# Kernel optimization log

Hardware: AMD Instinct MI355X
Metric: run time of the kernel (lower is better)

## Reference

```python
import jax, jax.numpy as jnp
import numpy as np

NEG_SLOPE = 0.2

def gatv2_conv(x, src, dst, Wl, Wr, att, b, num_nodes):
    # GATv2: e = att . leaky_relu(Wl x_src + Wr x_dst); segment softmax over dst; scatter-add of alpha * Wl x_src
    xl = x @ Wl  # [N, out]
    xr = x @ Wr  # [N, out]
    m = xl[src] + xr[dst]                        # [E, out] edge gather
    e = jax.nn.leaky_relu(m, NEG_SLOPE) @ att    # [E]
    emax = jax.ops.segment_max(e, dst, num_segments=num_nodes)
    ee = jnp.exp(e - emax[dst])
    denom = jax.ops.segment_sum(ee, dst, num_segments=num_nodes)
    alpha = ee / denom[dst]                      # [E]
    out = jax.ops.segment_sum(alpha[:, None] * xl[src], dst, num_segments=num_nodes)
    return out + b

def setup_inputs() -> dict:
    key = jax.random.key(0)
    ks = jax.random.split(key, 24)
    N, E, F, H, B = 40000, 640000, 128, 128, 64
    inp = {
        'x': jax.random.normal(ks[0], (N, F), dtype=jnp.float32),
        'edge_index': jax.random.randint(ks[1], (2, E), 0, N),
        'batch': jnp.sort(jax.random.randint(ks[2], (N,), 0, B)),
        'day': jax.random.randint(ks[3], (B,), 0, 7),
        'hour': jax.random.randint(ks[4], (B,), 0, 24),
    }
    def glorot(k, shape):
        lim = float(np.sqrt(6.0 / (shape[0] + shape[1])))
        return jax.random.uniform(k, shape, jnp.float32, -lim, lim)
    # GATv2 layers (heads=1)
    inp['Wl1'] = glorot(ks[5], (F, H)); inp['Wr1'] = glorot(ks[6], (F, H))
    inp['att1'] = glorot(ks[7], (H, 1))[:, 0]; inp['b1'] = jnp.zeros((H,), jnp.float32)
    inp['Wl2'] = glorot(ks[8], (H, H)); inp['Wr2'] = glorot(ks[9], (H, H))
    inp['att2'] = glorot(ks[10], (H, 1))[:, 0]; inp['b2'] = jnp.zeros((H,), jnp.float32)
    inp['Wl3'] = glorot(ks[11], (H, H)); inp['Wr3'] = glorot(ks[12], (H, H))
    inp['att3'] = glorot(ks[13], (H, 1))[:, 0]; inp['b3'] = jnp.zeros((H,), jnp.float32)
    # embeddings
    inp['day_tab'] = jax.random.normal(ks[14], (7, 64), dtype=jnp.float32)
    inp['hour_tab'] = jax.random.normal(ks[15], (24, 64), dtype=jnp.float32)
    # MLP head (weights stored [in, out])
    inp['W1'] = glorot(ks[16], (256, 256)); inp['bl1'] = jnp.zeros((256,), jnp.float32)
    inp['W2'] = glorot(ks[17], (256, 256)); inp['bl2'] = jnp.zeros((256,), jnp.float32)
    inp['W3'] = glorot(ks[18], (256, 1));   inp['bl3'] = jnp.zeros((1,), jnp.float32)
    return inp

def reference(x, edge_index, batch, day, hour,
              Wl1, Wr1, att1, b1, Wl2, Wr2, att2, b2, Wl3, Wr3, att3, b3,
              day_tab, hour_tab, W1, bl1, W2, bl2, W3, bl3):
    N = x.shape[0]
    B = day.shape[0]
    # add self loops (PyG default add_self_loops=True)
    loops = jnp.arange(N)
    src = jnp.concatenate([edge_index[0], loops])
    dst = jnp.concatenate([edge_index[1], loops])
    h = gatv2_conv(x, src, dst, Wl1, Wr1, att1, b1, N)
    h = jax.nn.relu(h)
    h = gatv2_conv(h, src, dst, Wl2, Wr2, att2, b2, N)
    h = jax.nn.relu(h)
    h = gatv2_conv(h, src, dst, Wl3, Wr3, att3, b3, N)
    # global mean pool over graphs
    sums = jax.ops.segment_sum(h, batch, num_segments=B)
    cnts = jax.ops.segment_sum(jnp.ones((N,), h.dtype), batch, num_segments=B)
    pooled = sums / jnp.maximum(cnts, 1.0)[:, None]      # [B, 128]
    feats = jnp.concatenate([pooled, day_tab[day], hour_tab[hour]], axis=1)  # [B, 256]
    z = jax.nn.relu(feats @ W1 + bl1)
    z = jax.nn.relu(z @ W2 + bl2)
    return z @ W3 + bl3  # [B, 1]
```

## Files before the change

### kernel.cpp

```cpp
#include <hip/hip_runtime.h>
#include <math.h>

#define NEG_SLOPE 0.2f
#define POOL_CHUNKS 8

typedef __attribute__((ext_vector_type(8))) short bf16x8;
typedef __attribute__((ext_vector_type(4))) float f32x4;

__device__ __forceinline__ void split_bf16(float x, short& hi, short& lo) {
    unsigned u = __float_as_uint(x);
    unsigned uh = u & 0xFFFF0000u;
    float r = x - __uint_as_float(uh);
    hi = (short)(uh >> 16);
    lo = (short)(__float_as_uint(r) >> 16);
}

__device__ __forceinline__ unsigned f2bf_rne(float x) {
    unsigned u = __float_as_uint(x);
    return (u + 0x7fffu + ((u >> 16) & 1u)) >> 16;
}

__global__ __launch_bounds__(256, 1) void node_gemm(
    const float* __restrict__ h, const float* __restrict__ Wl,
    const float* __restrict__ Wr, unsigned* __restrict__ xlb,
    float* __restrict__ xr, int N, int nTiles)
{
    const int w   = threadIdx.x >> 6;
    const int l   = threadIdx.x & 63;
    const int l15 = l & 15, lg = l >> 4;

    const float* __restrict__ Wsel = (w < 2) ? Wl : Wr;
    const int cbase = (w & 1) * 64;

    bf16x8 bh[4][4], bl_[4][4];
    #pragma unroll
    for (int ct = 0; ct < 4; ++ct) {
        const int c = cbase + ct * 16 + l15;
        #pragma unroll
        for (int kt = 0; kt < 4; ++kt) {
            #pragma unroll
            for (int i = 0; i < 8; ++i) {
                float v = Wsel[(kt * 32 + lg * 8 + i) * 128 + c];
                short hi, lo; split_bf16(v, hi, lo);
                bh[ct][kt][i] = hi; bl_[ct][kt][i] = lo;
            }
        }
    }

    for (int tile = blockIdx.x; tile < nTiles; tile += gridDim.x) {
        const int row0 = tile * 64;

        f32x4 acc[4][4];
        #pragma unroll
        for (int rt = 0; rt < 4; ++rt)
            #pragma unroll
            for (int ct = 0; ct < 4; ++ct)
                acc[rt][ct] = (f32x4){0.f, 0.f, 0.f, 0.f};

        #pragma unroll
        for (int rt = 0; rt < 4; ++rt) {
            int row = row0 + rt * 16 + l15;
            int rowc = row < N ? row : N - 1;
            bf16x8 ah[4], al[4];
            #pragma unroll
            for (int kt = 0; kt < 4; ++kt) {
                const float4 v0 = *(const float4*)&h[(size_t)rowc * 128 + kt * 32 + lg * 8];
                const float4 v1 = *(const float4*)&h[(size_t)rowc * 128 + kt * 32 + lg * 8 + 4];
                const float vv[8] = {v0.x, v0.y, v0.z, v0.w, v1.x, v1.y, v1.z, v1.w};
                #pragma unroll
                for (int i = 0; i < 8; ++i) {
                    short hi, lo; split_bf16(vv[i], hi, lo);
                    ah[kt][i] = hi; al[kt][i] = lo;
                }
            }
            #pragma unroll
            for (int kt = 0; kt < 4; ++kt) {
                #pragma unroll
                for (int ct = 0; ct < 4; ++ct) {
                    acc[rt][ct] = __builtin_amdgcn_mfma_f32_16x16x32_bf16(
                        ah[kt], bh[ct][kt], acc[rt][ct], 0, 0, 0);
                    acc[rt][ct] = __builtin_amdgcn_mfma_f32_16x16x32_bf16(
                        al[kt], bh[ct][kt], acc[rt][ct], 0, 0, 0);
                    acc[rt][ct] = __builtin_amdgcn_mfma_f32_16x16x32_bf16(
                        ah[kt], bl_[ct][kt], acc[rt][ct], 0, 0, 0);
                }
            }
        }

        if (w < 2) {
            #pragma unroll
            for (int rt = 0; rt < 4; ++rt) {
                #pragma unroll
                for (int ct = 0; ct < 4; ++ct) {
                    #pragma unroll
                    for (int j = 0; j < 4; ++j) {
                        int row = row0 + rt * 16 + lg * 4 + j;
                        unsigned o = f2bf_rne(acc[rt][ct][j]);
                        unsigned pr = (unsigned)__shfl_xor((int)o, 1);
                        if (!(l15 & 1) && row < N) {
                            int cp = (cbase + ct * 16 + l15) >> 1;
                            xlb[(size_t)row * 64 + cp] = o | (pr << 16);
                        }
                    }
                }
            }
        } else {
            #pragma unroll
            for (int rt = 0; rt < 4; ++rt) {
                #pragma unroll
                for (int ct = 0; ct < 4; ++ct) {
                    #pragma unroll
                    for (int j = 0; j < 4; ++j) {
                        int row = row0 + rt * 16 + lg * 4 + j;
                        if (row < N)
                            xr[(size_t)row * 128 + cbase + ct * 16 + l15] = acc[rt][ct][j];
                    }
                }
            }
        }
    }
}

__global__ __launch_bounds__(256) void zero_ints(int* __restrict__ p, int n)
{
    int i = blockIdx.x * blockDim.x + threadIdx.x;
    if (i < n) p[i] = 0;
}

__global__ __launch_bounds__(256) void edge_hist(
    const int* __restrict__ ei, int* __restrict__ deg, int E, int ET)
{
    int eid = blockIdx.x * blockDim.x + threadIdx.x;
    if (eid >= ET) return;
    int dst = (eid < E) ? ei[E + eid] : eid - E;
    atomicAdd(&deg[dst], 1);
}

__global__ __launch_bounds__(256) void scan_block(
    const int* __restrict__ in, int* __restrict__ out_excl,
    int* __restrict__ bsum, int N)
{
    __shared__ int sm[256];
    int t = threadIdx.x, i = blockIdx.x * 256 + t;
    int v = (i < N) ? in[i] : 0;
    sm[t] = v;
    __syncthreads();
    int x = v;
    for (int o = 1; o < 256; o <<= 1) {
        int u = (t >= o) ? sm[t - o] : 0;
        __syncthreads();
        x += u; sm[t] = x;
        __syncthreads();
    }
    if (i < N) out_excl[i] = x - v;
    if (t == 255) bsum[blockIdx.x] = x;
}

__global__ __launch_bounds__(256) void scan_sums(int* __restrict__ bsum, int nb)
{
    __shared__ int sm[256];
    int t = threadIdx.x;
    int v = (t < nb) ? bsum[t] : 0;
    sm[t] = v;
    __syncthreads();
    int x = v;
    for (int o = 1; o < 256; o <<= 1) {
        int u = (t >= o) ? sm[t - o] : 0;
        __syncthreads();
        x += u; sm[t] = x;
        __syncthreads();
    }
    if (t < nb) bsum[t] = x - v;
}

__global__ __launch_bounds__(256) void scan_final(
    const int* __restrict__ excl, const int* __restrict__ bsum,
    int* __restrict__ rowptr, int* __restrict__ cursor, int N, int ET)
{
    int i = blockIdx.x * blockDim.x + threadIdx.x;
    if (i > N) return;
    int v = (i < N) ? (excl[i] + bsum[i >> 8]) : ET;
    rowptr[i] = v;
    if (i < N) cursor[i] = v;
}

__global__ __launch_bounds__(256) void edge_fill(
    const int* __restrict__ ei, int* __restrict__ cursor,
    int* __restrict__ srcs, int E, int ET)
{
    int eid = blockIdx.x * blockDim.x + threadIdx.x;
    if (eid >= ET) return;
    int src, dst;
    if (eid < E) { src = ei[eid]; dst = ei[E + eid]; }
    else { src = dst = eid - E; }
    int pos = atomicAdd(&cursor[dst], 1);
    srcs[pos] = src;
}

__global__ __launch_bounds__(256) void gatv2_aggregate(
    const unsigned* __restrict__ xlb, const float* __restrict__ xr,
    const int* __restrict__ rowptr, const int* __restrict__ srcs,
    const float* __restrict__ att, const float* __restrict__ b,
    float* __restrict__ hout, int N, int do_relu)
{
    int n = blockIdx.x * 4 + (threadIdx.x >> 6);
    if (n >= N) return;
    const int lane = threadIdx.x & 63;
    const int hl = lane & 15;
    const int g  = lane >> 4;

    float xr8[8], at8[8];
    {
        const float4 a0 = *(const float4*)&xr[(size_t)n * 128 + hl * 8];
        const float4 a1 = *(const float4*)&xr[(size_t)n * 128 + hl * 8 + 4];
        xr8[0]=a0.x; xr8[1]=a0.y; xr8[2]=a0.z; xr8[3]=a0.w;
        xr8[4]=a1.x; xr8[5]=a1.y; xr8[6]=a1.z; xr8[7]=a1.w;
        const float4 t0 = *(const float4*)&att[hl * 8];
        const float4 t1 = *(const float4*)&att[hl * 8 + 4];
        at8[0]=t0.x; at8[1]=t0.y; at8[2]=t0.z; at8[3]=t0.w;
        at8[4]=t1.x; at8[5]=t1.y; at8[6]=t1.z; at8[7]=t1.w;
    }

    int r0 = rowptr[n], r1 = rowptr[n + 1];
    float m = -INFINITY, s = 0.f;
    float acc[8];
    #pragma unroll
    for (int c = 0; c < 8; ++c) acc[c] = 0.f;

    auto unpack = [&](const uint4 q, float* vv) {
        unsigned u;
        u = q.x; vv[0] = __uint_as_float(u << 16); vv[1] = __uint_as_float(u & 0xFFFF0000u);
        u = q.y; vv[2] = __uint_as_float(u << 16); vv[3] = __uint_as_float(u & 0xFFFF0000u);
        u = q.z; vv[4] = __uint_as_float(u << 16); vv[5] = __uint_as_float(u & 0xFFFF0000u);
        u = q.w; vv[6] = __uint_as_float(u << 16); vv[7] = __uint_as_float(u & 0xFFFF0000u);
    };
    auto score = [&](const float* vv) -> float {
        float p = 0.f;
        #pragma unroll
        for (int c = 0; c < 8; ++c) {
            float t = vv[c] + xr8[c];
            t = fmaxf(t, NEG_SLOPE * t);
            p += t * at8[c];
        }
        return p;
    };
    auto online = [&](float p, const float* vv) {
        float mn = fmaxf(m, p);
        float f = __expf(m - mn);
        float w = __expf(p - mn);
        s = s * f + w;
        #pragma unroll
        for (int c = 0; c < 8; ++c) acc[c] = acc[c] * f + w * vv[c];
        m = mn;
    };

    int j = r0 + g;
    int sa = (j < r1) ? srcs[j] : 0;
    int sb = (j + 4 < r1) ? srcs[j + 4] : sa;
    for (; j + 4 < r1; j += 8) {
        const uint4 qa = *(const uint4*)&xlb[(size_t)sa * 64 + hl * 4];
        const uint4 qb = *(const uint4*)&xlb[(size_t)sb * 64 + hl * 4];
        int jn0 = (j + 8  < r1) ? j + 8  : j;
        int jn1 = (j + 12 < r1) ? j + 12 : j;
        int sna = srcs[jn0], snb = srcs[jn1];
        float va[8], vb[8];
        unpack(qa, va); unpack(qb, vb);
        float pa = score(va), pb = score(vb);
        #pragma unroll
        for (int off = 1; off < 16; off <<= 1) {
            pa += __shfl_xor(pa, off);
            pb += __shfl_xor(pb, off);
        }
        online(pa, va);
        online(pb, vb);
        sa = sna; sb = snb;
    }
    if (j < r1) {
        const uint4 qa = *(const uint4*)&xlb[(size_t)sa * 64 + hl * 4];
        float va[8];
        unpack(qa, va);
        float pa = score(va);
        #pragma unroll
        for (int off = 1; off < 16; off <<= 1) pa += __shfl_xor(pa, off);
        online(pa, va);
    }

    float mm = m;
    mm = fmaxf(mm, __shfl_xor(mm, 16));
    mm = fmaxf(mm, __shfl_xor(mm, 32));
    float f = __expf(m - mm);
    s *= f;
    #pragma unroll
    for (int c = 0; c < 8; ++c) acc[c] *= f;
    s += __shfl_xor(s, 16); s += __shfl_xor(s, 32);
    #pragma unroll
    for (int c = 0; c < 8; ++c) {
        acc[c] += __shfl_xor(acc[c], 16);
        acc[c] += __shfl_xor(acc[c], 32);
    }

    if (g == 0) {
        float inv = 1.f / s;
        float o[8];
        #pragma unroll
        for (int c = 0; c < 8; ++c) {
            o[c] = acc[c] * inv + b[hl * 8 + c];
            if (do_relu) o[c] = fmaxf(o[c], 0.f);
        }
        *(float4*)&hout[(size_t)n * 128 + hl * 8]     = make_float4(o[0], o[1], o[2], o[3]);
        *(float4*)&hout[(size_t)n * 128 + hl * 8 + 4] = make_float4(o[4], o[5], o[6], o[7]);
    }
}

__global__ __launch_bounds__(256) void graph_bounds(
    const int* __restrict__ batch, int* __restrict__ gstart, int N, int B)
{
    int b = blockIdx.x * blockDim.x + threadIdx.x;
    if (b > B) return;
    int lo = 0, hi = N;
    while (lo < hi) {
        int mid = (lo + hi) >> 1;
        if (batch[mid] < b) lo = mid + 1; else hi = mid;
    }
    gstart[b] = lo;
}

__global__ __launch_bounds__(256) void pool_graph(
    const float* __restrict__ h, const int* __restrict__ gstart,
    float* __restrict__ pooled)
{
    __shared__ float sm[128];
    const int b = blockIdx.x / POOL_CHUNKS;
    const int chunk = blockIdx.x % POOL_CHUNKS;
    const int t = threadIdx.x;
    const int col = t & 127, hf = t >> 7;
    const int r0 = gstart[b], r1 = gstart[b + 1];
    const int len = r1 - r0;
    const int c0 = r0 + (int)(((long long)len * chunk) / POOL_CHUNKS);
    const int c1 = r0 + (int)(((long long)len * (chunk + 1)) / POOL_CHUNKS);
    float s = 0.f;
    for (int r = c0 + hf; r < c1; r += 2)
        s += h[(size_t)r * 128 + col];
    if (hf) sm[col] = s;
    __syncthreads();
    if (!hf) pooled[(size_t)(b * POOL_CHUNKS + chunk) * 128 + col] = s + sm[col];
}

__global__ __launch_bounds__(256) void mlp_head(
    const float* __restrict__ pooled, const int* __restrict__ gstart,
    const int* __restrict__ day, const int* __restrict__ hour,
    const float* __restrict__ day_tab, const float* __restrict__ hour_tab,
    const float* __restrict__ W1, const float* __restrict__ bl1,
    const float* __restrict__ W2, const float* __restrict__ bl2,
    const float* __restrict__ W3, const float* __restrict__ bl3,
    float* __restrict__ out)
{
    __shared__ float f0[256], f1[256];
    const int b = blockIdx.x, t = threadIdx.x;
    float c = fmaxf((float)(gstart[b + 1] - gstart[b]), 1.f);
    if (t < 128) {
        float sum = 0.f;
        #pragma unroll
        for (int ch = 0; ch < POOL_CHUNKS; ++ch)
            sum += pooled[(size_t)(b * POOL_CHUNKS + ch) * 128 + t];
        f0[t] = sum / c;
    }
    else if (t < 192) f0[t] = day_tab[day[b] * 64 + (t - 128)];
    else              f0[t] = hour_tab[hour[b] * 64 + (t - 192)];
    __syncthreads();
    float a = bl1[t];
    for (int k = 0; k < 256; ++k) a += f0[k] * W1[k * 256 + t];
    f1[t] = a > 0.f ? a : 0.f;
    __syncthreads();
    a = bl2[t];
    for (int k = 0; k < 256; ++k) a += f1[k] * W2[k * 256 + t];
    __syncthreads();
    f0[t] = a > 0.f ? a : 0.f;
    __syncthreads();
    f1[t] = f0[t] * W3[t];
    __syncthreads();
    for (int s2 = 128; s2 > 0; s2 >>= 1) {
        if (t < s2) f1[t] += f1[t + s2];
        __syncthreads();
    }
    if (t == 0) out[b] = f1[0] + bl3[0];
}

extern "C" void kernel_launch(void* const* d_in, const int* in_sizes, int n_in,
                              void* d_out, int out_size, void* d_ws, size_t ws_size,
                              hipStream_t stream) {
    const float* x        = (const float*)d_in[0];
    const int*   ei       = (const int*)d_in[1];
    const int*   batch    = (const int*)d_in[2];
    const int*   day      = (const int*)d_in[3];
    const int*   hour     = (const int*)d_in[4];
    const float* Wl[3]  = { (const float*)d_in[5],  (const float*)d_in[9],  (const float*)d_in[13] };
    const float* Wr[3]  = { (const float*)d_in[6],  (const float*)d_in[10], (const float*)d_in[14] };
    const float* att[3] = { (const float*)d_in[7],  (const float*)d_in[11], (const float*)d_in[15] };
    const float* bb[3]  = { (const float*)d_in[8],  (const float*)d_in[12], (const float*)d_in[16] };
    const float* day_tab  = (const float*)d_in[17];
    const float* hour_tab = (const float*)d_in[18];
    const float* W1 = (const float*)d_in[19]; const float* bl1 = (const float*)d_in[20];
    const float* W2 = (const float*)d_in[21]; const float* bl2 = (const float*)d_in[22];
    const float* W3 = (const float*)d_in[23]; const float* bl3 = (const float*)d_in[24];
    float* out = (float*)d_out;

    const int N  = in_sizes[0] / 128;
    const int E  = in_sizes[1] / 2;
    const int B  = in_sizes[3];
    const int ET = E + N;

    char* ws = (char*)d_ws;
    size_t off = 0;
    auto alloc = [&](size_t bytes) -> void* {
        void* p = ws + off;
        off += (bytes + 255) & ~(size_t)255;
        return p;
    };
    const size_t NB = (size_t)N * 128 * sizeof(float);
    unsigned* xlb = (unsigned*)alloc((size_t)N * 64 * sizeof(unsigned));
    float* xr     = (float*)alloc(NB);
    float* hbuf   = (float*)alloc(NB);
    int*   deg    = (int*)alloc((size_t)N * sizeof(int));
    int*   excl   = (int*)alloc((size_t)N * sizeof(int));
    int*   bsum   = (int*)alloc(256 * sizeof(int));
    int*   rowptr = (int*)alloc((size_t)(N + 1) * sizeof(int));
    int*   cursor = (int*)alloc((size_t)N * sizeof(int));
    int*   srcs   = (int*)alloc((size_t)ET * sizeof(int));
    int*   gstart = (int*)alloc((size_t)(B + 1) * sizeof(int));
    float* pooled = (float*)alloc((size_t)B * POOL_CHUNKS * 128 * sizeof(float));
    (void)ws_size;

    const int nb = (N + 255) / 256;
    const int edge_grid  = (ET + 255) / 256;
    const int node_grid4 = (N + 3) / 4;
    const int nTiles     = (N + 63) / 64;

    zero_ints<<<nb, 256, 0, stream>>>(deg, N);
    edge_hist<<<edge_grid, 256, 0, stream>>>(ei, deg, E, ET);
    scan_block<<<nb, 256, 0, stream>>>(deg, excl, bsum, N);
    scan_sums<<<1, 256, 0, stream>>>(bsum, nb);
    scan_final<<<(N + 256) / 256, 256, 0, stream>>>(excl, bsum, rowptr, cursor, N, ET);
    edge_fill<<<edge_grid, 256, 0, stream>>>(ei, cursor, srcs, E, ET);

    const float* hin = x;
    for (int l = 0; l < 3; ++l) {
        node_gemm<<<nTiles, 256, 0, stream>>>(hin, Wl[l], Wr[l], xlb, xr, N, nTiles);
        gatv2_aggregate<<<node_grid4, 256, 0, stream>>>(
            xlb, xr, rowptr, srcs, att[l], bb[l], hbuf, N, l < 2 ? 1 : 0);
        hin = hbuf;
    }

    graph_bounds<<<1, 256, 0, stream>>>(batch, gstart, N, B);
    pool_graph<<<B * POOL_CHUNKS, 256, 0, stream>>>(hbuf, gstart, pooled);
    mlp_head<<<B, 256, 0, stream>>>(pooled, gstart, day, hour, day_tab, hour_tab,
                                    W1, bl1, W2, bl2, W3, bl3, out);
}
```

Measured before the change: 298.8 us.

## Build CSR via two-level bucketed counting sort instead of per-node atomics

Replaces the per-destination histogram, three-kernel scan and per-node atomic fill with a two-level scheme. Edges are first counted and scattered into buckets of 32 destinations, packing src and the low bits of dst into one word. A per-bucket block then sorts locally in shared memory and writes rowptr and srcs. This cuts global atomic traffic and the number of scan launches, at the cost of an extra pass over the edges, a serial single-block bucket scan, and the assumption that src fits in 27 bits.

```diff
diff --git a/kernel.cpp b/kernel.cpp
--- a/kernel.cpp
+++ b/kernel.cpp
@@ -127,74 +127,90 @@
     if (i < n) p[i] = 0;
 }
 
-__global__ __launch_bounds__(256) void edge_hist(
-    const int* __restrict__ ei, int* __restrict__ deg, int E, int ET)
+__global__ __launch_bounds__(256) void bucket_hist(
+    const int* __restrict__ ei, int* __restrict__ bh, int E, int ET)
 {
     int eid = blockIdx.x * blockDim.x + threadIdx.x;
     if (eid >= ET) return;
     int dst = (eid < E) ? ei[E + eid] : eid - E;
-    atomicAdd(&deg[dst], 1);
-}
-
-__global__ __launch_bounds__(256) void scan_block(
-    const int* __restrict__ in, int* __restrict__ out_excl,
-    int* __restrict__ bsum, int N)
+    atomicAdd(&bh[dst >> 5], 1);
+}
+
+__global__ __launch_bounds__(256) void scan_buckets(
+    const int* __restrict__ bh, int* __restrict__ bbase,
+    int* __restrict__ bcursor, int* __restrict__ rowptr,
+    int NBK, int ET, int N)
 {
     __shared__ int sm[256];
-    int t = threadIdx.x, i = blockIdx.x * 256 + t;
-    int v = (i < N) ? in[i] : 0;
-    sm[t] = v;
-    __syncthreads();
-    int x = v;
-    for (int o = 1; o < 256; o <<= 1) {
-        int u = (t >= o) ? sm[t - o] : 0;
+    __shared__ int carry;
+    int t = threadIdx.x;
+    if (t == 0) carry = 0;
+    __syncthreads();
+    for (int c0 = 0; c0 < NBK; c0 += 256) {
+        int i = c0 + t;
+        int v = (i < NBK) ? bh[i] : 0;
+        sm[t] = v;
         __syncthreads();
-        x += u; sm[t] = x;
+        int x = v;
+        for (int o = 1; o < 256; o <<= 1) {
+            int u = (t >= o) ? sm[t - o] : 0;
+            __syncthreads();
+            x += u; sm[t] = x;
+            __syncthreads();
+        }
+        int excl = x - v + carry;
+        if (i < NBK) { bbase[i] = excl; bcursor[i] = excl; }
         __syncthreads();
-    }
-    if (i < N) out_excl[i] = x - v;
-    if (t == 255) bsum[blockIdx.x] = x;
-}
-
-__global__ __launch_bounds__(256) void scan_sums(int* __restrict__ bsum, int nb)
-{
-    __shared__ int sm[256];
-    int t = threadIdx.x;
-    int v = (t < nb) ? bsum[t] : 0;
-    sm[t] = v;
-    __syncthreads();
-    int x = v;
-    for (int o = 1; o < 256; o <<= 1) {
-        int u = (t >= o) ? sm[t - o] : 0;
+        if (t == 255) carry += x;
         __syncthreads();
-        x += u; sm[t] = x;
-        __syncthreads();
-    }
-    if (t < nb) bsum[t] = x - v;
-}
-
-__global__ __launch_bounds__(256) void scan_final(
-    const int* __restrict__ excl, const int* __restrict__ bsum,
-    int* __restrict__ rowptr, int* __restrict__ cursor, int N, int ET)
-{
-    int i = blockIdx.x * blockDim.x + threadIdx.x;
-    if (i > N) return;
-    int v = (i < N) ? (excl[i] + bsum[i >> 8]) : ET;
-    rowptr[i] = v;
-    if (i < N) cursor[i] = v;
-}
-
-__global__ __launch_bounds__(256) void edge_fill(
-    const int* __restrict__ ei, int* __restrict__ cursor,
-    int* __restrict__ srcs, int E, int ET)
+    }
+    if (t == 0) { bbase[NBK] = ET; rowptr[N] = ET; }
+}
+
+__global__ __launch_bounds__(256) void bucket_scatter(
+    const int* __restrict__ ei, int* __restrict__ bcursor,
+    unsigned* __restrict__ sbuf, int E, int ET)
 {
     int eid = blockIdx.x * blockDim.x + threadIdx.x;
     if (eid >= ET) return;
     int src, dst;
     if (eid < E) { src = ei[eid]; dst = ei[E + eid]; }
     else { src = dst = eid - E; }
-    int pos = atomicAdd(&cursor[dst], 1);
-    srcs[pos] = src;
+    int pos = atomicAdd(&bcursor[dst >> 5], 1);
+    sbuf[pos] = ((unsigned)src << 5) | (unsigned)(dst & 31);
+}
+
+__global__ __launch_bounds__(128) void bucket_sort(
+    const unsigned* __restrict__ sbuf, const int* __restrict__ bbase,
+    int* __restrict__ rowptr, int* __restrict__ srcs, int N)
+{
+    __shared__ int hist[32];
+    __shared__ int cur[32];
+    const int k = blockIdx.x;
+    const int t = threadIdx.x;
+    const int b0 = bbase[k], b1 = bbase[k + 1];
+    if (t < 32) hist[t] = 0;
+    __syncthreads();
+    for (int i = b0 + t; i < b1; i += 128)
+        atomicAdd(&hist[sbuf[i] & 31u], 1);
+    __syncthreads();
+    if (t == 0) {
+        int run = 0;
+        #pragma unroll
+        for (int d = 0; d < 32; ++d) {
+            int c = hist[d];
+            cur[d] = run;
+            int dst = k * 32 + d;
+            if (dst < N) rowptr[dst] = b0 + run;
+            run += c;
+        }
+    }
+    __syncthreads();
+    for (int i = b0 + t; i < b1; i += 128) {
+        unsigned u = sbuf[i];
+        int pos = atomicAdd(&cur[u & 31u], 1);
+        srcs[b0 + pos] = (int)(u >> 5);
+    }
 }
 
 __global__ __launch_bounds__(256) void gatv2_aggregate(
@@ -409,6 +425,7 @@
     const int E  = in_sizes[1] / 2;
     const int B  = in_sizes[3];
     const int ET = E + N;
+    const int NBK = (N + 31) / 32;
 
     char* ws = (char*)d_ws;
     size_t off = 0;
@@ -418,30 +435,28 @@
         return p;
     };
     const size_t NB = (size_t)N * 128 * sizeof(float);
-    unsigned* xlb = (unsigned*)alloc((size_t)N * 64 * sizeof(unsigned));
-    float* xr     = (float*)alloc(NB);
-    float* hbuf   = (float*)alloc(NB);
-    int*   deg    = (int*)alloc((size_t)N * sizeof(int));
-    int*   excl   = (int*)alloc((size_t)N * sizeof(int));
-    int*   bsum   = (int*)alloc(256 * sizeof(int));
-    int*   rowptr = (int*)alloc((size_t)(N + 1) * sizeof(int));
-    int*   cursor = (int*)alloc((size_t)N * sizeof(int));
-    int*   srcs   = (int*)alloc((size_t)ET * sizeof(int));
-    int*   gstart = (int*)alloc((size_t)(B + 1) * sizeof(int));
-    float* pooled = (float*)alloc((size_t)B * POOL_CHUNKS * 128 * sizeof(float));
+    unsigned* xlb   = (unsigned*)alloc((size_t)N * 64 * sizeof(unsigned));
+    float* xr       = (float*)alloc(NB);
+    float* hbuf     = (float*)alloc(NB);
+    int*   bh       = (int*)alloc((size_t)(NBK + 1) * sizeof(int));
+    int*   bbase    = (int*)alloc((size_t)(NBK + 1) * sizeof(int));
+    int*   bcursor  = (int*)alloc((size_t)NBK * sizeof(int));
+    unsigned* sbuf  = (unsigned*)alloc((size_t)ET * sizeof(unsigned));
+    int*   rowptr   = (int*)alloc((size_t)(N + 1) * sizeof(int));
+    int*   srcs     = (int*)alloc((size_t)ET * sizeof(int));
+    int*   gstart   = (int*)alloc((size_t)(B + 1) * sizeof(int));
+    float* pooled   = (float*)alloc((size_t)B * POOL_CHUNKS * 128 * sizeof(float));
     (void)ws_size;
 
-    const int nb = (N + 255) / 256;
     const int edge_grid  = (ET + 255) / 256;
     const int node_grid4 = (N + 3) / 4;
     const int nTiles     = (N + 63) / 64;
 
-    zero_ints<<<nb, 256, 0, stream>>>(deg, N);
-    edge_hist<<<edge_grid, 256, 0, stream>>>(ei, deg, E, ET);
-    scan_block<<<nb, 256, 0, stream>>>(deg, excl, bsum, N);
-    scan_sums<<<1, 256, 0, stream>>>(bsum, nb);
-    scan_final<<<(N + 256) / 256, 256, 0, stream>>>(excl, bsum, rowptr, cursor, N, ET);
-    edge_fill<<<edge_grid, 256, 0, stream>>>(ei, cursor, srcs, E, ET);
+    zero_ints<<<(NBK + 256) / 256, 256, 0, stream>>>(bh, NBK + 1);
+    bucket_hist<<<edge_grid, 256, 0, stream>>>(ei, bh, E, ET);
+    scan_buckets<<<1, 256, 0, stream>>>(bh, bbase, bcursor, rowptr, NBK, ET, N);
+    bucket_scatter<<<edge_grid, 256, 0, stream>>>(ei, bcursor, sbuf, E, ET);
+    bucket_sort<<<NBK, 128, 0, stream>>>(sbuf, bbase, rowptr, srcs, N);
 
     const float* hin = x;
     for (int l = 0; l < 3; ++l) {
```

Measured after the change: 490.4 us. 1.64x slower.
